# Kernel tuning notes

Measured on AMD Instinct MI355X. Metric: run time of the kernel, lower is better.

## Reference

```python
import jax, jax.numpy as jnp
import numpy as np

N = 50000        # nodes
E = 800000       # edges
D_IN = 64        # input_dim
D_E = 16         # edge_dim
D_OUT = 64       # output_dim
HEADS = 8
HEAD_DIM = D_OUT // HEADS
COMB = 2 * D_IN + D_E  # 144


def _linear_init(key, fan_in, fan_out):
    kw, kb = jax.random.split(key)
    lim = 1.0 / np.sqrt(fan_in)
    W = jax.random.uniform(kw, (fan_in, fan_out), minval=-lim, maxval=lim, dtype=jnp.float32)
    b = jax.random.uniform(kb, (fan_out,), minval=-lim, maxval=lim, dtype=jnp.float32)
    return W, b


def setup_inputs() -> dict:
    key = jax.random.key(0)
    ks = jax.random.split(key, 16)
    inp = {
        "x": jax.random.normal(ks[0], (N, D_IN), dtype=jnp.float32),
        "edge_attr": jax.random.normal(ks[1], (E, D_E), dtype=jnp.float32),
        "edge_index": jax.random.randint(ks[2], (2, E), 0, N, dtype=jnp.int32),
        "q": jax.random.uniform(ks[3], (1, D_OUT), dtype=jnp.float32) * 0.1,
    }
    # three ResidualStacks: k (COMB->D_OUT), v (COMB->D_OUT), out (D_OUT->D_OUT)
    for pre, fan_in, kbase in (("k", COMB, 4), ("v", COMB, 8), ("o", D_OUT, 12)):
        W0, b0 = _linear_init(ks[kbase], fan_in, D_OUT)
        W1, b1 = _linear_init(ks[kbase + 1], D_OUT, D_OUT)
        W2, b2 = _linear_init(ks[kbase + 2], D_OUT, D_OUT)
        inp.update({f"{pre}_W0": W0, f"{pre}_b0": b0,
                    f"{pre}_W1": W1, f"{pre}_b1": b1,
                    f"{pre}_W2": W2, f"{pre}_b2": b2})
    return inp


def residual_stack(h, W0, b0, W1, b1, W2, b2, last_activation):
    # input projection + ReLU, then 2 residual linear blocks
    h = jax.nn.relu(h @ W0 + b0)
    h = jax.nn.relu(h + h @ W1 + b1)
    h = h + h @ W2 + b2
    if last_activation:
        h = jax.nn.relu(h)
    return h


def neighborhood_attention(q, k, v, index):
    # q: (1, D_OUT), k/v: (E, D_OUT), index: (E,) destination node ids
    kh = k.reshape(E, HEADS, HEAD_DIM)
    qh = q.reshape(1, HEADS, HEAD_DIM)
    scores = jnp.sum(qh * kh, axis=-1) / np.sqrt(HEAD_DIM)  # (E, HEADS)
    m = jax.ops.segment_max(scores, index, num_segments=N)  # (N, HEADS)
    ex = jnp.exp(scores - jax.lax.stop_gradient(m)[index])
    denom = jax.ops.segment_sum(ex, index, num_segments=N)  # (N, HEADS)
    alpha = ex / denom[index]
    vh = v.reshape(E, HEADS, HEAD_DIM)
    return (alpha[:, :, None] * vh).reshape(E, D_OUT)


def reference(x, edge_attr, edge_index, q,
              k_W0, k_b0, k_W1, k_b1, k_W2, k_b2,
              v_W0, v_b0, v_W1, v_b1, v_W2, v_b2,
              o_W0, o_b0, o_W1, o_b1, o_W2, o_b2):
    src, dst = edge_index[0], edge_index[1]
    feat = jnp.concatenate([x[src], x[dst], edge_attr], axis=-1)  # (E, COMB)
    k = residual_stack(feat, k_W0, k_b0, k_W1, k_b1, k_W2, k_b2, last_activation=False)
    v = residual_stack(feat, v_W0, v_b0, v_W1, v_b1, v_W2, v_b2, last_activation=False)
    messages = neighborhood_attention(q, k, v, dst)               # (E, D_OUT)
    aggr = jax.ops.segment_sum(messages, dst, num_segments=N)    # (N, D_OUT)
    out = residual_stack(jax.nn.relu(aggr), o_W0, o_b0, o_W1, o_b1, o_W2, o_b2, last_activation=False)
    # skip_connection=True, input_dim == output_dim -> identity skip
    return jax.nn.relu(x + out)
```

## Files before the change

kernel.cpp:

```cpp
#include <hip/hip_runtime.h>

#define N_NODES 50000
#define E_EDGES 800000
#define D_OUT   64
#define COMB    144

typedef float  f32x4  __attribute__((ext_vector_type(4)));
typedef __bf16 bf16x8 __attribute__((ext_vector_type(8)));
typedef __bf16 bf16x4 __attribute__((ext_vector_type(4)));

#define WS_DEG     0
#define WS_START   200064
#define WS_CURSOR  400128
#define WS_WTS     600192
#define WS_PERM    707840
#define WS_MSG     3907840

#define BIG_ELEMS    (64*168)
#define SMALL_ELEMS  (64*72)

__global__ __launch_bounds__(256) void prep_kernel(
    const float* __restrict__ kW0, const float* __restrict__ kW1, const float* __restrict__ kW2,
    const float* __restrict__ vW0, const float* __restrict__ vW1, const float* __restrict__ vW2,
    const float* __restrict__ oW0, const float* __restrict__ oW1, const float* __restrict__ oW2,
    __bf16* __restrict__ wout)
{
    const int b = blockIdx.x, tid = threadIdx.x;
    const float* src;
    __bf16* dst;
    int K, Kpad, lb;
    if (b < 42)      { src = kW0; dst = wout;             K = 144; Kpad = 168; lb = b; }
    else if (b < 84) { src = vW0; dst = wout + BIG_ELEMS; K = 144; Kpad = 168; lb = b - 42; }
    else {
        const int id = (b - 84) / 18; lb = (b - 84) % 18;
        const float* s7[7] = {kW1, kW2, vW1, vW2, oW0, oW1, oW2};
        src = s7[id]; dst = wout + 2 * BIG_ELEMS + id * SMALL_ELEMS;
        K = 64; Kpad = 72;
    }
    const int idx = lb * 256 + tid;
    const int col = idx / Kpad, k = idx % Kpad;
    dst[idx] = (k < K) ? (__bf16)src[k * 64 + col] : (__bf16)0.f;
}

__global__ __launch_bounds__(256) void deg_kernel(const int* __restrict__ edge_index,
                                                  int* __restrict__ deg)
{
    const int e = blockIdx.x * 256 + threadIdx.x;
    if (e < E_EDGES) atomicAdd(&deg[edge_index[E_EDGES + e]], 1);
}

__global__ __launch_bounds__(1024) void scan_kernel(const int* __restrict__ deg,
                                                    int* __restrict__ start,
                                                    int* __restrict__ cursor)
{
    __shared__ int wsum[16];
    __shared__ int carry_s;
    const int tid = threadIdx.x, lane = tid & 63, wv = tid >> 6;
    if (tid == 0) carry_s = 0;
    __syncthreads();
    for (int base = 0; base < N_NODES; base += 1024) {
        const int i = base + tid;
        const int v = (i < N_NODES) ? deg[i] : 0;
        int sc = v;
        #pragma unroll
        for (int off = 1; off < 64; off <<= 1) {
            int t = __shfl_up(sc, off);
            if (lane >= off) sc += t;
        }
        if (lane == 63) wsum[wv] = sc;
        const int c = carry_s;
        __syncthreads();
        if (wv == 0 && lane < 16) {
            int ws = wsum[lane];
            #pragma unroll
            for (int off = 1; off < 16; off <<= 1) {
                int t = __shfl_up(ws, off);
                if (lane >= off) ws += t;
            }
            wsum[lane] = ws;
        }
        __syncthreads();
        const int woff = (wv == 0) ? 0 : wsum[wv - 1];
        const int excl = c + woff + sc - v;
        if (i < N_NODES) { start[i] = excl; cursor[i] = excl; }
        __syncthreads();
        if (tid == 0) carry_s = c + wsum[15];
        __syncthreads();
    }
}

__global__ __launch_bounds__(256) void perm_kernel(const int* __restrict__ edge_index,
                                                   int* __restrict__ cursor,
                                                   int* __restrict__ perm)
{
    const int e = blockIdx.x * 256 + threadIdx.x;
    if (e < E_EDGES) {
        const int d = edge_index[E_EDGES + e];
        perm[atomicAdd(&cursor[d], 1)] = e;
    }
}

__device__ __forceinline__ void gemm64(const __bf16* Arow, const __bf16* Wt,
                                       int hi, int row16, f32x4 acc[4])
{
    #pragma unroll
    for (int kc = 0; kc < 2; ++kc) {
        const bf16x8 a = *(const bf16x8*)(Arow + kc * 32 + hi * 8);
        #pragma unroll
        for (int n = 0; n < 4; ++n) {
            const bf16x8 bfr = *(const bf16x8*)(Wt + (n * 16 + row16) * 72 + kc * 32 + hi * 8);
            acc[n] = __builtin_amdgcn_mfma_f32_16x16x32_bf16(a, bfr, acc[n], 0, 0, 0);
        }
    }
}

__device__ __forceinline__ bf16x8 pack8(float4 a, float4 b) {
    bf16x8 r;
    r[0] = (__bf16)a.x; r[1] = (__bf16)a.y; r[2] = (__bf16)a.z; r[3] = (__bf16)a.w;
    r[4] = (__bf16)b.x; r[5] = (__bf16)b.y; r[6] = (__bf16)b.z; r[7] = (__bf16)b.w;
    return r;
}

__global__ __launch_bounds__(256, 5) void edge_kernel(
    const float* __restrict__ x,
    const float* __restrict__ edge_attr,
    const int*   __restrict__ edge_index,
    const float* __restrict__ q,
    const float* __restrict__ kb0, const float* __restrict__ kb1, const float* __restrict__ kb2,
    const float* __restrict__ vb0, const float* __restrict__ vb1, const float* __restrict__ vb2,
    const __bf16* __restrict__ kW0t, const __bf16* __restrict__ kW1t, const __bf16* __restrict__ kW2t,
    const __bf16* __restrict__ vW0t, const __bf16* __restrict__ vW1t, const __bf16* __restrict__ vW2t,
    __bf16* __restrict__ msg)
{
    __shared__ __bf16 HK_s[64][72];
    __shared__ __bf16 HV_s[64][72];

    const int tid   = threadIdx.x;
    const int lane  = tid & 63;
    const int w     = tid >> 6;
    const int row16 = lane & 15;
    const int hi    = lane >> 4;
    const int wrow  = w * 16;

    const int e0 = (blockIdx.x * 4 + w) * 16;
    const int er = e0 + row16;

    const int src  = edge_index[er];
    const int dstn = edge_index[E_EDGES + er];

    bf16x8 af[5];
    {
        const float* xs = &x[(size_t)src * 64 + hi * 8];
        af[0] = pack8(*(const float4*)xs,        *(const float4*)(xs + 4));
        af[1] = pack8(*(const float4*)(xs + 32), *(const float4*)(xs + 36));
        const float* xd = &x[(size_t)dstn * 64 + hi * 8];
        af[2] = pack8(*(const float4*)xd,        *(const float4*)(xd + 4));
        af[3] = pack8(*(const float4*)(xd + 32), *(const float4*)(xd + 36));
        if (hi < 2) {
            const float* ep = &edge_attr[(size_t)er * 16 + hi * 8];
            af[4] = pack8(*(const float4*)ep, *(const float4*)(ep + 4));
        } else {
            #pragma unroll
            for (int i = 0; i < 8; ++i) af[4][i] = (__bf16)0.f;
        }
    }

    const __bf16* hrowK = &HK_s[wrow + row16][0];
    const __bf16* hrowV = &HV_s[wrow + row16][0];

    float h0K[4][4], h0V[4][4];
    {
        f32x4 aK[4] = {{0,0,0,0},{0,0,0,0},{0,0,0,0},{0,0,0,0}};
        f32x4 aV[4] = {{0,0,0,0},{0,0,0,0},{0,0,0,0},{0,0,0,0}};
        #pragma unroll
        for (int kc = 0; kc < 5; ++kc) {
            #pragma unroll
            for (int n = 0; n < 4; ++n) {
                const bf16x8 bK = *(const bf16x8*)(kW0t + (n * 16 + row16) * 168 + kc * 32 + hi * 8);
                aK[n] = __builtin_amdgcn_mfma_f32_16x16x32_bf16(af[kc], bK, aK[n], 0, 0, 0);
                const bf16x8 bV = *(const bf16x8*)(vW0t + (n * 16 + row16) * 168 + kc * 32 + hi * 8);
                aV[n] = __builtin_amdgcn_mfma_f32_16x16x32_bf16(af[kc], bV, aV[n], 0, 0, 0);
            }
        }
        #pragma unroll
        for (int n = 0; n < 4; ++n) {
            const float bK = kb0[n * 16 + row16];
            const float bV = vb0[n * 16 + row16];
            #pragma unroll
            for (int r = 0; r < 4; ++r) {
                h0K[n][r] = fmaxf(aK[n][r] + bK, 0.f);
                h0V[n][r] = fmaxf(aV[n][r] + bV, 0.f);
                HK_s[wrow + hi * 4 + r][n * 16 + row16] = (__bf16)h0K[n][r];
                HV_s[wrow + hi * 4 + r][n * 16 + row16] = (__bf16)h0V[n][r];
            }
        }
    }
    __builtin_amdgcn_wave_barrier();

    float h1K[4][4], h1V[4][4];
    {
        f32x4 cK[4] = {{0,0,0,0},{0,0,0,0},{0,0,0,0},{0,0,0,0}};
        f32x4 cV[4] = {{0,0,0,0},{0,0,0,0},{0,0,0,0},{0,0,0,0}};
        gemm64(hrowK, kW1t, hi, row16, cK);
        gemm64(hrowV, vW1t, hi, row16, cV);
        #pragma unroll
        for (int n = 0; n < 4; ++n) {
            const float bK = kb1[n * 16 + row16];
            const float bV = vb1[n * 16 + row16];
            #pragma unroll
            for (int r = 0; r < 4; ++r) {
                h1K[n][r] = fmaxf(h0K[n][r] + cK[n][r] + bK, 0.f);
                h1V[n][r] = fmaxf(h0V[n][r] + cV[n][r] + bV, 0.f);
                HK_s[wrow + hi * 4 + r][n * 16 + row16] = (__bf16)h1K[n][r];
                HV_s[wrow + hi * 4 + r][n * 16 + row16] = (__bf16)h1V[n][r];
            }
        }
    }
    __builtin_amdgcn_wave_barrier();

    {
        f32x4 cK[4] = {{0,0,0,0},{0,0,0,0},{0,0,0,0},{0,0,0,0}};
        f32x4 cV[4] = {{0,0,0,0},{0,0,0,0},{0,0,0,0},{0,0,0,0}};
        gemm64(hrowK, kW2t, hi, row16, cK);
        gemm64(hrowV, vW2t, hi, row16, cV);

        float ex[4][4], vv[4][4];
        #pragma unroll
        for (int n = 0; n < 4; ++n) {
            const float bK = kb2[n * 16 + row16];
            const float bV = vb2[n * 16 + row16];
            const float qv = q[n * 16 + row16];
            #pragma unroll
            for (int r = 0; r < 4; ++r) {
                const float kk = h1K[n][r] + cK[n][r] + bK;
                vv[n][r] = h1V[n][r] + cV[n][r] + bV;
                float p2 = qv * kk;
                p2 += __shfl_xor(p2, 1);
                p2 += __shfl_xor(p2, 2);
                p2 += __shfl_xor(p2, 4);
                ex[n][r] = __expf(p2 * 0.35355339059327373f);
            }
        }

        #pragma unroll
        for (int r = 0; r < 4; ++r) {
            __bf16* mrow = msg + (size_t)(e0 + hi * 4 + r) * 72;
            #pragma unroll
            for (int n = 0; n < 4; ++n)
                mrow[n * 16 + row16] = (__bf16)(ex[n][r] * vv[n][r]);
            if ((row16 & 7) == 0) {
                #pragma unroll
                for (int n = 0; n < 4; ++n)
                    mrow[64 + 2 * n + (row16 >> 3)] = (__bf16)ex[n][r];
            }
        }
    }
}

__global__ __launch_bounds__(256, 8) void aggr_kernel(
    const int* __restrict__ start, const int* __restrict__ endc,
    const int* __restrict__ perm, const __bf16* __restrict__ msg,
    float* __restrict__ aggr_out)
{
    const int lane = threadIdx.x & 63;
    const int n    = blockIdx.x * 4 + (threadIdx.x >> 6);
    if (n >= N_NODES) return;
    const int g = lane >> 4;
    const int l = lane & 15;
    const int s0 = start[n], e1 = endc[n];

    float m0 = 0.f, m1 = 0.f, m2 = 0.f, m3 = 0.f, ae = 0.f;
    for (int i = s0 + g; i < e1; i += 4) {
        const size_t b0 = (size_t)perm[i] * 72;
        const bf16x4 v = *(const bf16x4*)&msg[b0 + l * 4];
        ae += (float)msg[b0 + 64 + (l >> 1)];
        m0 += (float)v[0]; m1 += (float)v[1]; m2 += (float)v[2]; m3 += (float)v[3];
    }
    #pragma unroll
    for (int m = 16; m < 64; m <<= 1) {
        m0 += __shfl_xor(m0, m); m1 += __shfl_xor(m1, m);
        m2 += __shfl_xor(m2, m); m3 += __shfl_xor(m3, m);
        ae += __shfl_xor(ae, m);
    }
    if (g == 0) {
        const float inv = (ae > 0.f) ? 1.f / ae : 0.f;
        float4 o;
        o.x = fmaxf(m0 * inv, 0.f);
        o.y = fmaxf(m1 * inv, 0.f);
        o.z = fmaxf(m2 * inv, 0.f);
        o.w = fmaxf(m3 * inv, 0.f);
        *(float4*)&aggr_out[(size_t)n * 64 + l * 4] = o;
    }
}

__global__ __launch_bounds__(256) void node_kernel(
    const float* __restrict__ x, const float* __restrict__ aggr_in,
    const float* __restrict__ ob0, const float* __restrict__ ob1, const float* __restrict__ ob2,
    const __bf16* __restrict__ oW0t, const __bf16* __restrict__ oW1t, const __bf16* __restrict__ oW2t,
    float* __restrict__ out)
{
    __shared__ __bf16 A_s[64][72];
    __shared__ __bf16 H_s[64][72];

    const int tid  = threadIdx.x;
    const int lane = tid & 63;
    const int w    = tid >> 6;
    const int n0   = blockIdx.x * 64;
    const int row16 = lane & 15;
    const int hi    = lane >> 4;

    {
        const int r = tid >> 2, seg = tid & 3;
        const int node = n0 + r;
        #pragma unroll
        for (int gg = 0; gg < 4; ++gg) {
            bf16x4 h; h[0] = h[1] = h[2] = h[3] = (__bf16)0.f;
            if (node < N_NODES) {
                const float4 f = *(const float4*)&aggr_in[(size_t)node * 64 + seg * 16 + gg * 4];
                h[0] = (__bf16)f.x; h[1] = (__bf16)f.y; h[2] = (__bf16)f.z; h[3] = (__bf16)f.w;
            }
            *(bf16x4*)&A_s[r][seg * 16 + gg * 4] = h;
        }
    }
    __syncthreads();

    const __bf16* arow = &A_s[w * 16 + row16][0];
    const __bf16* hrow = &H_s[w * 16 + row16][0];

    f32x4 acc[4] = {{0,0,0,0},{0,0,0,0},{0,0,0,0},{0,0,0,0}};
    gemm64(arow, oW0t, hi, row16, acc);
    float h0[4][4];
    #pragma unroll
    for (int n = 0; n < 4; ++n) {
        const float bias = ob0[n * 16 + row16];
        #pragma unroll
        for (int r = 0; r < 4; ++r) {
            h0[n][r] = fmaxf(acc[n][r] + bias, 0.f);
            H_s[w * 16 + hi * 4 + r][n * 16 + row16] = (__bf16)h0[n][r];
        }
    }
    __builtin_amdgcn_wave_barrier();

    f32x4 acc1[4] = {{0,0,0,0},{0,0,0,0},{0,0,0,0},{0,0,0,0}};
    gemm64(hrow, oW1t, hi, row16, acc1);
    float h1[4][4];
    #pragma unroll
    for (int n = 0; n < 4; ++n) {
        const float bias = ob1[n * 16 + row16];
        #pragma unroll
        for (int r = 0; r < 4; ++r) {
            h1[n][r] = fmaxf(h0[n][r] + acc1[n][r] + bias, 0.f);
            H_s[w * 16 + hi * 4 + r][n * 16 + row16] = (__bf16)h1[n][r];
        }
    }
    __builtin_amdgcn_wave_barrier();

    f32x4 acc2[4] = {{0,0,0,0},{0,0,0,0},{0,0,0,0},{0,0,0,0}};
    gemm64(hrow, oW2t, hi, row16, acc2);
    #pragma unroll
    for (int n = 0; n < 4; ++n) {
        const float bias = ob2[n * 16 + row16];
        #pragma unroll
        for (int r = 0; r < 4; ++r) {
            const int node = n0 + w * 16 + hi * 4 + r;
            if (node < N_NODES) {
                const int col = n * 16 + row16;
                const float o = h1[n][r] + acc2[n][r] + bias;
                out[(size_t)node * 64 + col] = fmaxf(x[(size_t)node * 64 + col] + o, 0.f);
            }
        }
    }
}

extern "C" void kernel_launch(void* const* d_in, const int* in_sizes, int n_in,
                              void* d_out, int out_size, void* d_ws, size_t ws_size,
                              hipStream_t stream) {
    const float* x  = (const float*)d_in[0];
    const float* ea = (const float*)d_in[1];
    const int*   ei = (const int*)d_in[2];
    const float* q  = (const float*)d_in[3];
    const float* kW0 = (const float*)d_in[4];  const float* kb0 = (const float*)d_in[5];
    const float* kW1 = (const float*)d_in[6];  const float* kb1 = (const float*)d_in[7];
    const float* kW2 = (const float*)d_in[8];  const float* kb2 = (const float*)d_in[9];
    const float* vW0 = (const float*)d_in[10]; const float* vb0 = (const float*)d_in[11];
    const float* vW1 = (const float*)d_in[12]; const float* vb1 = (const float*)d_in[13];
    const float* vW2 = (const float*)d_in[14]; const float* vb2 = (const float*)d_in[15];
    const float* oW0 = (const float*)d_in[16]; const float* ob0 = (const float*)d_in[17];
    const float* oW1 = (const float*)d_in[18]; const float* ob1 = (const float*)d_in[19];
    const float* oW2 = (const float*)d_in[20]; const float* ob2 = (const float*)d_in[21];

    char* ws = (char*)d_ws;
    int*    deg    = (int*)(ws + WS_DEG);
    int*    start  = (int*)(ws + WS_START);
    int*    cursor = (int*)(ws + WS_CURSOR);
    __bf16* wts    = (__bf16*)(ws + WS_WTS);
    int*    perm   = (int*)(ws + WS_PERM);
    __bf16* msg    = (__bf16*)(ws + WS_MSG);
    float*  aggrf  = (float*)d_out;

    __bf16* kW0t = wts;
    __bf16* vW0t = wts + BIG_ELEMS;
    __bf16* sm   = wts + 2 * BIG_ELEMS;
    __bf16* kW1t = sm;                   __bf16* kW2t = sm + SMALL_ELEMS;
    __bf16* vW1t = sm + 2 * SMALL_ELEMS; __bf16* vW2t = sm + 3 * SMALL_ELEMS;
    __bf16* oW0t = sm + 4 * SMALL_ELEMS; __bf16* oW1t = sm + 5 * SMALL_ELEMS;
    __bf16* oW2t = sm + 6 * SMALL_ELEMS;

    hipMemsetAsync(deg, 0, (size_t)N_NODES * sizeof(int), stream);

    deg_kernel<<<E_EDGES / 256, 256, 0, stream>>>(ei, deg);
    scan_kernel<<<1, 1024, 0, stream>>>(deg, start, cursor);
    perm_kernel<<<E_EDGES / 256, 256, 0, stream>>>(ei, cursor, perm);

    prep_kernel<<<210, 256, 0, stream>>>(kW0, kW1, kW2, vW0, vW1, vW2, oW0, oW1, oW2, wts);

    edge_kernel<<<E_EDGES / 64, 256, 0, stream>>>(
        x, ea, ei, q,
        kb0, kb1, kb2, vb0, vb1, vb2,
        kW0t, kW1t, kW2t, vW0t, vW1t, vW2t,
        msg);

    aggr_kernel<<<(N_NODES + 3) / 4, 256, 0, stream>>>(start, cursor, perm, msg, aggrf);

    node_kernel<<<(N_NODES + 63) / 64, 256, 0, stream>>>(
        x, aggrf, ob0, ob1, ob2, oW0t, oW1t, oW2t, (float*)d_out);
}
```

Before: 475.0 us.

## Split message buffer into value and exp arrays, widen aggregation loads

The interleaved 72-wide bf16 message rows become two arrays: a 64-wide value array and an 8-wide per-head exp-sum array. The aggregation kernel now has 8 lanes per edge, each loading 16-byte bf16x8 vectors, and processes 8 edges per wavefront iteration instead of 4. The edge kernel's minimum-occupancy hint rises from 5 to 6 waves. The aim is aligned, wider gathers in the bandwidth-bound scatter-aggregate step. The costs are two scattered accesses per edge, more accumulator registers, and possible register spilling in the edge kernel under the tighter bound.

```diff
diff --git a/kernel.cpp b/kernel.cpp
--- a/kernel.cpp
+++ b/kernel.cpp
@@ -14,7 +14,8 @@
 #define WS_CURSOR  400128
 #define WS_WTS     600192
 #define WS_PERM    707840
-#define WS_MSG     3907840
+#define WS_VMSG    3907840
+#define WS_EXMSG   106307840
 
 #define BIG_ELEMS    (64*168)
 #define SMALL_ELEMS  (64*72)
@@ -121,7 +122,7 @@
     return r;
 }
 
-__global__ __launch_bounds__(256, 5) void edge_kernel(
+__global__ __launch_bounds__(256, 6) void edge_kernel(
     const float* __restrict__ x,
     const float* __restrict__ edge_attr,
     const int*   __restrict__ edge_index,
@@ -130,7 +131,7 @@
     const float* __restrict__ vb0, const float* __restrict__ vb1, const float* __restrict__ vb2,
     const __bf16* __restrict__ kW0t, const __bf16* __restrict__ kW1t, const __bf16* __restrict__ kW2t,
     const __bf16* __restrict__ vW0t, const __bf16* __restrict__ vW1t, const __bf16* __restrict__ vW2t,
-    __bf16* __restrict__ msg)
+    __bf16* __restrict__ vmsg, __bf16* __restrict__ exmsg)
 {
     __shared__ __bf16 HK_s[64][72];
     __shared__ __bf16 HV_s[64][72];
@@ -244,14 +245,16 @@
 
         #pragma unroll
         for (int r = 0; r < 4; ++r) {
-            __bf16* mrow = msg + (size_t)(e0 + hi * 4 + r) * 72;
+            const int erow = e0 + hi * 4 + r;
+            __bf16* mrow = vmsg + (size_t)erow * 64;
             #pragma unroll
             for (int n = 0; n < 4; ++n)
                 mrow[n * 16 + row16] = (__bf16)(ex[n][r] * vv[n][r]);
             if ((row16 & 7) == 0) {
+                __bf16* erow8 = exmsg + (size_t)erow * 8;
                 #pragma unroll
                 for (int n = 0; n < 4; ++n)
-                    mrow[64 + 2 * n + (row16 >> 3)] = (__bf16)ex[n][r];
+                    erow8[2 * n + (row16 >> 3)] = (__bf16)ex[n][r];
             }
         }
     }
@@ -259,37 +262,41 @@
 
 __global__ __launch_bounds__(256, 8) void aggr_kernel(
     const int* __restrict__ start, const int* __restrict__ endc,
-    const int* __restrict__ perm, const __bf16* __restrict__ msg,
+    const int* __restrict__ perm,
+    const __bf16* __restrict__ vmsg, const __bf16* __restrict__ exmsg,
     float* __restrict__ aggr_out)
 {
     const int lane = threadIdx.x & 63;
     const int n    = blockIdx.x * 4 + (threadIdx.x >> 6);
     if (n >= N_NODES) return;
-    const int g = lane >> 4;
-    const int l = lane & 15;
+    const int g = lane >> 3;
+    const int l = lane & 7;
     const int s0 = start[n], e1 = endc[n];
 
-    float m0 = 0.f, m1 = 0.f, m2 = 0.f, m3 = 0.f, ae = 0.f;
-    for (int i = s0 + g; i < e1; i += 4) {
-        const size_t b0 = (size_t)perm[i] * 72;
-        const bf16x4 v = *(const bf16x4*)&msg[b0 + l * 4];
-        ae += (float)msg[b0 + 64 + (l >> 1)];
-        m0 += (float)v[0]; m1 += (float)v[1]; m2 += (float)v[2]; m3 += (float)v[3];
+    float m[8] = {0.f, 0.f, 0.f, 0.f, 0.f, 0.f, 0.f, 0.f};
+    float ae = 0.f;
+    for (int i = s0 + g; i < e1; i += 8) {
+        const int pe = perm[i];
+        const bf16x8 v = *(const bf16x8*)&vmsg[(size_t)pe * 64 + l * 8];
+        ae += (float)exmsg[(size_t)pe * 8 + l];
+        #pragma unroll
+        for (int j = 0; j < 8; ++j) m[j] += (float)v[j];
     }
     #pragma unroll
-    for (int m = 16; m < 64; m <<= 1) {
-        m0 += __shfl_xor(m0, m); m1 += __shfl_xor(m1, m);
-        m2 += __shfl_xor(m2, m); m3 += __shfl_xor(m3, m);
-        ae += __shfl_xor(ae, m);
+    for (int mask = 8; mask < 64; mask <<= 1) {
+        #pragma unroll
+        for (int j = 0; j < 8; ++j) m[j] += __shfl_xor(m[j], mask);
+        ae += __shfl_xor(ae, mask);
     }
     if (g == 0) {
         const float inv = (ae > 0.f) ? 1.f / ae : 0.f;
-        float4 o;
-        o.x = fmaxf(m0 * inv, 0.f);
-        o.y = fmaxf(m1 * inv, 0.f);
-        o.z = fmaxf(m2 * inv, 0.f);
-        o.w = fmaxf(m3 * inv, 0.f);
-        *(float4*)&aggr_out[(size_t)n * 64 + l * 4] = o;
+        float4 o0, o1;
+        o0.x = fmaxf(m[0] * inv, 0.f); o0.y = fmaxf(m[1] * inv, 0.f);
+        o0.z = fmaxf(m[2] * inv, 0.f); o0.w = fmaxf(m[3] * inv, 0.f);
+        o1.x = fmaxf(m[4] * inv, 0.f); o1.y = fmaxf(m[5] * inv, 0.f);
+        o1.z = fmaxf(m[6] * inv, 0.f); o1.w = fmaxf(m[7] * inv, 0.f);
+        *(float4*)&aggr_out[(size_t)n * 64 + l * 8]     = o0;
+        *(float4*)&aggr_out[(size_t)n * 64 + l * 8 + 4] = o1;
     }
 }
 
@@ -395,7 +402,8 @@
     int*    cursor = (int*)(ws + WS_CURSOR);
     __bf16* wts    = (__bf16*)(ws + WS_WTS);
     int*    perm   = (int*)(ws + WS_PERM);
-    __bf16* msg    = (__bf16*)(ws + WS_MSG);
+    __bf16* vmsg   = (__bf16*)(ws + WS_VMSG);
+    __bf16* exmsg  = (__bf16*)(ws + WS_EXMSG);
     float*  aggrf  = (float*)d_out;
 
     __bf16* kW0t = wts;
@@ -418,9 +426,9 @@
         x, ea, ei, q,
         kb0, kb1, kb2, vb0, vb1, vb2,
         kW0t, kW1t, kW2t, vW0t, vW1t, vW2t,
-        msg);
-
-    aggr_kernel<<<(N_NODES + 3) / 4, 256, 0, stream>>>(start, cursor, perm, msg, aggrf);
+        vmsg, exmsg);
+
+    aggr_kernel<<<(N_NODES + 3) / 4, 256, 0, stream>>>(start, cursor, perm, vmsg, exmsg, aggrf);
 
     node_kernel<<<(N_NODES + 63) / 64, 256, 0, stream>>>(
         x, aggrf, ob0, ob1, ob2, oW0t, oW1t, oW2t, (float*)d_out);
```

After: 523.1 us. +10.1%, slower.
